# Kernel optimization log

Hardware: AMD Instinct MI355X
Metric: run time of the kernel (lower is better)

## Reference

```python
import jax, jax.numpy as jnp
import numpy as np

E = 512   # embed_dim == decoder_dim (structurally required by the module)
D = 512
V = 10000
B = 64
S = 32    # encoded caption length; max decode steps T = S - 1


def _lstm_cell(x, h, c, wih, whh, bih, bhh):
    # torch.nn.LSTMCell gate order: i, f, g, o
    gates = x @ wih.T + h @ whh.T + bih + bhh
    i, f, g, o = jnp.split(gates, 4, axis=-1)
    c2 = jax.nn.sigmoid(f) * c + jax.nn.sigmoid(i) * jnp.tanh(g)
    h2 = jax.nn.sigmoid(o) * jnp.tanh(c2)
    return h2, c2


def setup_inputs() -> dict:
    key = jax.random.key(0)
    ks = jax.random.split(key, 16)
    encoder_out = jax.random.normal(ks[0], (B, E), jnp.float32)
    encoded_captions = jax.random.randint(ks[1], (B, S), 0, V)
    # lengths sorted descending (required by the ragged :batch_size_t slicing); force max = S
    lens = np.sort(np.asarray(jax.random.randint(ks[2], (B,), 8, S + 1)))[::-1].copy()
    lens[0] = S
    caption_lengths = jnp.asarray(lens, jnp.int32)
    u = lambda k, sh: jax.random.uniform(k, sh, jnp.float32, -0.1, 0.1)
    return {
        'encoder_out': encoder_out,
        'encoded_captions': encoded_captions,
        'caption_lengths': caption_lengths,
        'embedding': u(ks[3], (V, E)),
        'dec_wih': u(ks[4], (4 * D, 2 * E)),
        'dec_whh': u(ks[5], (4 * D, D)),
        'dec_bih': u(ks[6], (4 * D,)),
        'dec_bhh': u(ks[7], (4 * D,)),
        'w_wih': u(ks[8], (4, E)),
        'w_whh': u(ks[9], (4, 1)),
        'w_bih': u(ks[10], (4,)),
        'w_bhh': u(ks[11], (4,)),
        'init_h_w': u(ks[12], (1, E)),
        'init_h_b': jnp.zeros((1,), jnp.float32),
        'init_c_w': u(ks[13], (1, E)),
        'init_c_b': jnp.zeros((1,), jnp.float32),
        'cls_w': u(ks[14], (V, D)),
        'cls_b': jnp.zeros((V,), jnp.float32),
    }


def reference(encoder_out, encoded_captions, caption_lengths, embedding,
              dec_wih, dec_whh, dec_bih, dec_bhh,
              w_wih, w_whh, w_bih, w_bhh,
              init_h_w, init_h_b, init_c_w, init_c_b,
              cls_w, cls_b):
    dl = caption_lengths - 1                      # decode lengths, [B]
    T = int(np.max(np.asarray(dl)))
    emb = embedding[encoded_captions]             # [B,S,E]
    xs = jnp.moveaxis(emb[:, :T, :], 1, 0)        # [T,B,E]
    wh0 = encoder_out @ init_h_w.T + init_h_b     # [B,1]
    wc0 = encoder_out @ init_c_w.T + init_c_b     # [B,1]

    def step(carry, inp):
        t, x_e = inp
        h, c, wh, wc = carry
        m = (dl > t).astype(x_e.dtype)[:, None]   # [B,1] active-row mask (ragged batch)
        wh2, wc2 = _lstm_cell(encoder_out, wh, wc, w_wih, w_whh, w_bih, w_bhh)
        x = jnp.concatenate([x_e, encoder_out], axis=-1)           # [B,2E]
        h2, c2 = _lstm_cell(x, h, c, dec_wih, dec_whh, dec_bih, dec_bhh)
        preds = (h2 @ cls_w.T + cls_b) * m        # inactive rows stay 0 (dropout is eval-mode identity)
        wgt = jax.nn.sigmoid(wh2)[:, 0] * m[:, 0] # [B]
        keep = m > 0
        carry = (jnp.where(keep, h2, h), jnp.where(keep, c2, c),
                 jnp.where(keep, wh2, wh), jnp.where(keep, wc2, wc))
        return carry, (preds, wgt)

    carry0 = (encoder_out, encoder_out, wh0, wc0)
    _, (p_seq, w_seq) = jax.lax.scan(step, carry0, (jnp.arange(T), xs))
    predictions = jnp.moveaxis(p_seq, 0, 1)                        # [B,T,V]
    weights = jnp.broadcast_to(w_seq.T[:, :, None], (B, T, V))     # replicate per-step scalar across vocab
    return predictions, dl, weights
```

## Files before the change

kernel.cpp:

```cpp
#include <hip/hip_runtime.h>
#include <hip/hip_bf16.h>


typedef __attribute__((ext_vector_type(4))) float f32x4;
typedef __attribute__((ext_vector_type(8))) short short8;
typedef __attribute__((ext_vector_type(4))) unsigned short u16x4;

#define BB 64
#define SS 32
#define TT 31
#define EE 512
#define VV 10000

__device__ __forceinline__ float sigf(float x){ return 1.0f/(1.0f + __expf(-x)); }
__device__ __forceinline__ float tanh_(float x){
  x = fminf(15.f, fmaxf(-15.f, x));
  float e = __expf(2.f*x);
  return (e-1.f)/(e+1.f);
}
__device__ __forceinline__ unsigned short f2bf(float x){
  __hip_bfloat16 h = __float2bfloat16(x);
  return __builtin_bit_cast(unsigned short, h);
}
__device__ __forceinline__ short8 cvt8(f32x4 a, f32x4 b){
  short8 t;
  t[0] = (short)f2bf(a.x); t[1] = (short)f2bf(a.y);
  t[2] = (short)f2bf(a.z); t[3] = (short)f2bf(a.w);
  t[4] = (short)f2bf(b.x); t[5] = (short)f2bf(b.y);
  t[6] = (short)f2bf(b.z); t[7] = (short)f2bf(b.w);
  return t;
}
__device__ __forceinline__ short8 ld16_coh(const void* p){
  short8 r;
  asm volatile("global_load_dwordx4 %0, %1, off sc0 sc1" : "=v"(r) : "v"(p) : "memory");
  return r;
}
__device__ __forceinline__ void st8_coh(void* p, unsigned long long v){
  asm volatile("global_store_dwordx2 %0, %1, off sc0 sc1" :: "v"(p), "v"(v) : "memory");
}

#define NPREP 2048
__global__ __launch_bounds__(256) void k_prep(
    const float* __restrict__ dwih, const float* __restrict__ dwhh,
    const float* __restrict__ emb, const int* __restrict__ cap,
    const float* __restrict__ enc,
    __hip_bfloat16* __restrict__ wihbf, __hip_bfloat16* __restrict__ whhbf,
    __hip_bfloat16* __restrict__ xa, __hip_bfloat16* __restrict__ h0,
    const int* __restrict__ caplen,
    const float* __restrict__ wwih, const float* __restrict__ wwhh,
    const float* __restrict__ wbih, const float* __restrict__ wbhh,
    const float* __restrict__ ihw, const float* __restrict__ ihb,
    const float* __restrict__ icw, const float* __restrict__ icb,
    float* __restrict__ wgt, unsigned* __restrict__ flags,
    float* __restrict__ dl_out)
{
  if (blockIdx.x >= NPREP){
    int b = blockIdx.x - NPREP;
    int w = threadIdx.x >> 6, lane = threadIdx.x & 63;
    __shared__ float sv[6];

    float p = 0.f;
    for (int k = lane; k < EE; k += 64) p += enc[b*EE + k] * wwih[w*EE + k];
    #pragma unroll
    for (int off = 32; off; off >>= 1) p += __shfl_down(p, off, 64);
    if (lane == 0) sv[w] = p;

    if (w < 2){
      const float* iw = (w == 0) ? ihw : icw;
      float q = 0.f;
      for (int k = lane; k < EE; k += 64) q += enc[b*EE + k] * iw[k];
      #pragma unroll
      for (int off = 32; off; off >>= 1) q += __shfl_down(q, off, 64);
      if (lane == 0) sv[4 + w] = q + ((w == 0) ? ihb[0] : icb[0]);
    }
    __syncthreads();

    if (threadIdx.x == 0){
      float wh = sv[4], wc = sv[5];
      int dl = caplen[b] - 1;
      for (int t = 0; t < TT; t++){
        float gi = sv[0] + wh*wwhh[0] + wbih[0] + wbhh[0];
        float gf = sv[1] + wh*wwhh[1] + wbih[1] + wbhh[1];
        float gg = sv[2] + wh*wwhh[2] + wbih[2] + wbhh[2];
        float go = sv[3] + wh*wwhh[3] + wbih[3] + wbhh[3];
        float wc2 = sigf(gf)*wc + sigf(gi)*tanh_(gg);
        float wh2 = sigf(go)*tanh_(wc2);
        float m = (dl > t) ? 1.f : 0.f;
        wgt[b*TT + t] = sigf(wh2) * m;
        if (dl > t){ wh = wh2; wc = wc2; }
      }
      dl_out[b] = (float)dl;
    }
    if (b == 0) for (int i = threadIdx.x; i < 4096; i += 256) flags[i] = 0;
    return;
  }

  const int n1 = 262144;
  const int n2 = n1 + 131072;
  const int n3 = n2 + 253952;
  const int n4 = n3 + 4096;
  for (int i = blockIdx.x*blockDim.x + threadIdx.x; i < n4; i += NPREP*256){
    const float* src; __hip_bfloat16* dst;
    if (i < n1){ src = dwih + (size_t)i*8; dst = wihbf + (size_t)i*8; }
    else if (i < n2){ int j = i - n1; src = dwhh + (size_t)j*8; dst = whhbf + (size_t)j*8; }
    else if (i < n3){
      int j = i - n2; int e = j*8;
      int r = e >> 10, k = e & 1023, t = r >> 6, b = r & 63;
      src = (k < 512) ? emb + (size_t)cap[b*SS + t]*EE + k
                      : enc + (size_t)b*EE + (k - 512);
      dst = xa + (size_t)e;
    } else {
      int j = i - n3; int e = j*8;
      src = enc + (size_t)e; dst = h0 + (size_t)e;
    }
    f32x4 lo = *(const f32x4*)src;
    f32x4 hi = *(const f32x4*)(src + 4);
    *(short8*)dst = cvt8(lo, hi);
  }
}

__global__ __launch_bounds__(256) void k_xproj(
    const __hip_bfloat16* __restrict__ xa, const __hip_bfloat16* __restrict__ wihbf,
    const float* __restrict__ bih, const float* __restrict__ bhh,
    float* __restrict__ xp)
{
  int bm = blockIdx.y;
  int bn = blockIdx.x;
  int w = threadIdx.x >> 6, lane = threadIdx.x & 63;
  int col = lane & 15, kg = lane >> 4;
  int m0 = bm*64;
  int n0 = bn*256 + w*64;

  f32x4 acc[4][4] = {};
  for (int kk = 0; kk < 32; kk++){
    short8 aW[4], aX[4];
    #pragma unroll
    for (int i = 0; i < 4; i++){
      aW[i] = *(const short8*)(wihbf + (size_t)(n0 + i*16 + col)*1024 + kk*32 + kg*8);
      aX[i] = *(const short8*)(xa    + (size_t)(m0 + i*16 + col)*1024 + kk*32 + kg*8);
    }
    #pragma unroll
    for (int nt = 0; nt < 4; nt++)
      #pragma unroll
      for (int mt = 0; mt < 4; mt++)
        acc[nt][mt] = __builtin_amdgcn_mfma_f32_16x16x32_bf16(aW[nt], aX[mt], acc[nt][mt], 0, 0, 0);
  }
  #pragma unroll
  for (int nt = 0; nt < 4; nt++){
    int n = n0 + nt*16 + 4*kg;
    f32x4 badd = *(const f32x4*)(bih + n);
    f32x4 b2   = *(const f32x4*)(bhh + n);
    badd = badd + b2;
    #pragma unroll
    for (int mt = 0; mt < 4; mt++){
      int r = m0 + mt*16 + col;
      *(f32x4*)(xp + (size_t)r*2048 + n) = acc[nt][mt] + badd;
    }
  }
}

__global__ __launch_bounds__(64, 1) void k_rec(
    const __hip_bfloat16* __restrict__ whhbf,
    const float* __restrict__ xp,
    const float* __restrict__ enc,
    const int* __restrict__ caplen,
    char* __restrict__ hbuf,
    __hip_bfloat16* __restrict__ hout,
    unsigned* __restrict__ flags,
    const float* __restrict__ clsw,
    __hip_bfloat16* __restrict__ clsbf)
{
  const int bid = blockIdx.x;
  const int lane = threadIdx.x;

  if (bid >= 128){
    const int n4 = 1280000;
    for (int i = (bid - 128)*64 + lane; i < n4; i += 384*64){
      f32x4 v = ((const f32x4*)clsw)[i];
      u16x4 o;
      o.x = f2bf(v.x); o.y = f2bf(v.y); o.z = f2bf(v.z); o.w = f2bf(v.w);
      ((u16x4*)clsbf)[i] = o;
    }
    return;
  }

  const int g = bid >> 5, s = bid & 31;
  const int col = lane & 15, kg = lane >> 4;
  const int d0 = s*16;
  const int b  = g*16 + col;
  const int dbase = d0 + 4*kg;
  const int pme = (dbase >> 2);

  short8 Aq[4][16];
  #pragma unroll
  for (int q = 0; q < 4; q++){
    const __hip_bfloat16* wrow = whhbf + (size_t)(q*512 + d0 + col)*512;
    #pragma unroll
    for (int kk = 0; kk < 16; kk++)
      Aq[q][kk] = *(const short8*)(wrow + kk*32 + kg*8);
  }
  #pragma unroll
  for (int q = 0; q < 4; q++)
    #pragma unroll
    for (int kk = 0; kk < 16; kk++)
      asm volatile("" : "+v"(Aq[q][kk]));

  float hst[4], cst[4];
  #pragma unroll
  for (int j = 0; j < 4; j++){
    float e0 = enc[(size_t)b*EE + dbase + j];
    hst[j] = e0; cst[j] = e0;
  }
  const int dl = caplen[b] - 1;
  unsigned* myflag = flags + (size_t)(g*32 + s)*32;
  const unsigned* pollflag = flags + (size_t)(g*32 + (lane & 31))*32;

  f32x4 xg[4];
  #pragma unroll
  for (int q = 0; q < 4; q++)
    xg[q] = *(const f32x4*)(xp + (size_t)b*2048 + q*512 + dbase);

  for (int t = 0; t < TT; t++){
    if (t > 0){
      const unsigned tgt = (unsigned)t;
      while (1){
        unsigned v = __hip_atomic_load(pollflag, __ATOMIC_RELAXED, __HIP_MEMORY_SCOPE_AGENT);
        v = min(v, (unsigned)__shfl_xor((int)v, 1, 64));
        v = min(v, (unsigned)__shfl_xor((int)v, 2, 64));
        v = min(v, (unsigned)__shfl_xor((int)v, 4, 64));
        v = min(v, (unsigned)__shfl_xor((int)v, 8, 64));
        v = min(v, (unsigned)__shfl_xor((int)v, 16, 64));
        if (v >= tgt) break;
        __builtin_amdgcn_s_sleep(1);
      }
    }

    const char* hc = hbuf + (size_t)(t & 1)*65536 + (size_t)b*1024 + kg*16;
    short8 Bf[16];
    #pragma unroll
    for (int kk = 0; kk < 16; kk++)
      Bf[kk] = ld16_coh(hc + kk*64);

    f32x4 xgn[4];
    if (t + 1 < TT){
      #pragma unroll
      for (int q = 0; q < 4; q++)
        xgn[q] = *(const f32x4*)(xp + (size_t)((t+1)*BB + b)*2048 + q*512 + dbase);
    }

    asm volatile("s_waitcnt vmcnt(0)" ::: "memory");
    __builtin_amdgcn_sched_barrier(0);

    f32x4 acc[4] = {};
    #pragma unroll
    for (int kk = 0; kk < 16; kk++)
      #pragma unroll
      for (int q = 0; q < 4; q++)
        acc[q] = __builtin_amdgcn_mfma_f32_16x16x32_bf16(Aq[q][kk], Bf[kk], acc[q], 0, 0, 0);

    const bool act = dl > t;
    unsigned long long hpack = 0, spack = 0;
    #pragma unroll
    for (int j = 0; j < 4; j++){
      float gi = acc[0][j] + xg[0][j];
      float gf = acc[1][j] + xg[1][j];
      float gg = acc[2][j] + xg[2][j];
      float go = acc[3][j] + xg[3][j];
      float c2 = sigf(gf)*cst[j] + sigf(gi)*tanh_(gg);
      float h2 = sigf(go)*tanh_(c2);
      if (act){ cst[j] = c2; hst[j] = h2; }
      hpack |= (unsigned long long)f2bf(h2)     << (16*j);
      spack |= (unsigned long long)f2bf(hst[j]) << (16*j);
    }

    ((unsigned long long*)hout)[((size_t)b*TT + t)*128 + pme] = hpack;

    if (t < TT - 1){
      st8_coh(hbuf + (size_t)((t + 1) & 1)*65536 + (size_t)b*1024 + (size_t)dbase*2, spack);
      asm volatile("s_waitcnt vmcnt(0)" ::: "memory");
      if (lane == 0)
        __hip_atomic_store(myflag, (unsigned)(t + 1),
                           __ATOMIC_RELAXED, __HIP_MEMORY_SCOPE_AGENT);
    }

    #pragma unroll
    for (int q = 0; q < 4; q++) xg[q] = xgn[q];
  }
}

__global__ __launch_bounds__(256) void k_cls(
    const __hip_bfloat16* __restrict__ hbf,
    const __hip_bfloat16* __restrict__ wbf,
    const float* __restrict__ clsb,
    const float* __restrict__ wgt,
    float* __restrict__ preds, float* __restrict__ wout)
{
  int bid = blockIdx.x;
  if (bid >= 1264){
    int r = bid - 1264;
    float wv = wgt[r];
    f32x4 wq = {wv, wv, wv, wv};
    f32x4* dst = (f32x4*)(wout + (size_t)r*VV);
    #pragma unroll 2
    for (int i = threadIdx.x; i < VV/4; i += 256)
      dst[i] = wq;
    return;
  }

  int bn = bid % 79, bm = bid / 79;
  int w = threadIdx.x >> 6, lane = threadIdx.x & 63;
  int col = lane & 15, kg = lane >> 4;
  int m0 = bm*128 + (w >> 1)*64;
  int n0 = bn*128 + (w & 1)*64;
  if (m0 >= 1984) return;

  int arow[4], brow[4];
  #pragma unroll
  for (int i = 0; i < 4; i++){
    arow[i] = min(m0 + i*16 + col, 1983);
    brow[i] = min(n0 + i*16 + col, 9999);
  }
  f32x4 acc[4][4] = {};
  for (int kk = 0; kk < 16; kk++){
    short8 a[4], b[4];
    #pragma unroll
    for (int i = 0; i < 4; i++){
      a[i] = *(const short8*)(hbf + (size_t)arow[i]*512 + kk*32 + kg*8);
      b[i] = *(const short8*)(wbf + (size_t)brow[i]*512 + kk*32 + kg*8);
    }
    #pragma unroll
    for (int mt = 0; mt < 4; mt++)
      #pragma unroll
      for (int nt = 0; nt < 4; nt++)
        acc[mt][nt] = __builtin_amdgcn_mfma_f32_16x16x32_bf16(a[mt], b[nt], acc[mt][nt], 0, 0, 0);
  }
  float cb[4]; int vcol[4]; bool vok[4];
  #pragma unroll
  for (int nt = 0; nt < 4; nt++){
    int v = n0 + nt*16 + col; vcol[nt] = v; vok[nt] = (v < VV);
    cb[nt] = vok[nt] ? clsb[v] : 0.f;
  }
  #pragma unroll
  for (int mt = 0; mt < 4; mt++)
    #pragma unroll
    for (int rg = 0; rg < 4; rg++){
      int r = m0 + mt*16 + 4*kg + rg;
      if (r >= 1984) continue;
      float wv = wgt[r];
      float mf = (wv > 0.f) ? 1.f : 0.f;
      size_t base = (size_t)r*VV;
      #pragma unroll
      for (int nt = 0; nt < 4; nt++){
        if (!vok[nt]) continue;
        preds[base + vcol[nt]] = (acc[mt][nt][rg] + cb[nt]) * mf;
      }
    }
}

extern "C" void kernel_launch(void* const* d_in, const int* in_sizes, int n_in,
                              void* d_out, int out_size, void* d_ws, size_t ws_size,
                              hipStream_t stream) {
  const float* enc    = (const float*)d_in[0];
  const int*   cap    = (const int*)  d_in[1];
  const int*   caplen = (const int*)  d_in[2];
  const float* emb    = (const float*)d_in[3];
  const float* dwih   = (const float*)d_in[4];
  const float* dwhh   = (const float*)d_in[5];
  const float* dbih   = (const float*)d_in[6];
  const float* dbhh   = (const float*)d_in[7];
  const float* wwih   = (const float*)d_in[8];
  const float* wwhh   = (const float*)d_in[9];
  const float* wbih   = (const float*)d_in[10];
  const float* wbhh   = (const float*)d_in[11];
  const float* ihw    = (const float*)d_in[12];
  const float* ihb    = (const float*)d_in[13];
  const float* icw    = (const float*)d_in[14];
  const float* icb    = (const float*)d_in[15];
  const float* clsw   = (const float*)d_in[16];
  const float* clsb   = (const float*)d_in[17];

  float* preds  = (float*)d_out;
  float* dl_out = preds + (size_t)BB*TT*VV;
  float* wout   = dl_out + BB;

  char* ws = (char*)d_ws;
  float*          wgt   = (float*)         (ws + 0);
  unsigned*       flags = (unsigned*)      (ws + 8192);
  __hip_bfloat16* clsbf = (__hip_bfloat16*)(ws + 24576);
  __hip_bfloat16* wihbf = (__hip_bfloat16*)(ws + 10264576);
  __hip_bfloat16* whhbf = (__hip_bfloat16*)(ws + 14458880);
  __hip_bfloat16* xa    = (__hip_bfloat16*)(ws + 16556032);
  float*          xp    = (float*)         (ws + 20619264);
  char*           hbuf  = (char*)          (ws + 36872192);
  __hip_bfloat16* hout  = (__hip_bfloat16*)(ws + 37003264);

  k_prep <<<NPREP + BB, 256, 0, stream>>>(dwih, dwhh, emb, cap, enc,
                                          wihbf, whhbf, xa,
                                          (__hip_bfloat16*)hbuf,
                                          caplen, wwih, wwhh, wbih, wbhh,
                                          ihw, ihb, icw, icb, wgt, flags, dl_out);
  k_xproj<<<dim3(8, 31), 256, 0, stream>>>(xa, wihbf, dbih, dbhh, xp);
  k_rec  <<<512, 64, 0, stream>>>(whhbf, xp, enc, caplen, hbuf, hout, flags,
                                  clsw, clsbf);
  k_cls  <<<1264 + 1984, 256, 0, stream>>>(hout, clsbf, clsb, wgt, preds, wout);
}
```

Baseline: 284.1 us.

## Stage classifier GEMM tiles through padded LDS with register prefetch

The classifier GEMM now loads 128x64 bf16 tiles of the activations and weights cooperatively into padded shared memory, then reads MFMA fragments from LDS instead of each wave fetching its own fragments straight from global memory. The next K-slice is prefetched into registers while the current one is computed. This cuts redundant global loads across waves and gives more coalesced access, at the cost of two barriers per K-step and more LDS use. The early return for out-of-range waves moves after the loop, since every thread now has to reach the barriers.

New measurement: 258.3 us. 1.1x faster.

```diff
diff --git a/kernel.cpp b/kernel.cpp
--- a/kernel.cpp
+++ b/kernel.cpp
@@ -307,38 +307,71 @@
     return;
   }
 
+  __shared__ __hip_bfloat16 Ab[128*72];
+  __shared__ __hip_bfloat16 Bb[128*72];
+
   int bn = bid % 79, bm = bid / 79;
-  int w = threadIdx.x >> 6, lane = threadIdx.x & 63;
+  int tid = threadIdx.x;
+  int w = tid >> 6, lane = tid & 63;
   int col = lane & 15, kg = lane >> 4;
+
+  int srow[4], skseg[4]; const __hip_bfloat16 *gA[4], *gB[4];
+  #pragma unroll
+  for (int j = 0; j < 4; j++){
+    int s = j*256 + tid;
+    srow[j] = s & 127; skseg[j] = s >> 7;
+    gA[j] = hbf + (size_t)min(bm*128 + srow[j], 1983)*512 + skseg[j]*8;
+    gB[j] = wbf + (size_t)min(bn*128 + srow[j], 9999)*512 + skseg[j]*8;
+  }
+
+  f32x4 acc[4][4] = {};
+  short8 rA[4], rB[4];
+  #pragma unroll
+  for (int j = 0; j < 4; j++){
+    rA[j] = *(const short8*)(gA[j]);
+    rB[j] = *(const short8*)(gB[j]);
+  }
+
+  for (int bk = 0; bk < 8; bk++){
+    __syncthreads();
+    #pragma unroll
+    for (int j = 0; j < 4; j++){
+      *(short8*)(Ab + srow[j]*72 + skseg[j]*8) = rA[j];
+      *(short8*)(Bb + srow[j]*72 + skseg[j]*8) = rB[j];
+    }
+    __syncthreads();
+    if (bk < 7){
+      #pragma unroll
+      for (int j = 0; j < 4; j++){
+        rA[j] = *(const short8*)(gA[j] + (bk+1)*64);
+        rB[j] = *(const short8*)(gB[j] + (bk+1)*64);
+      }
+    }
+    #pragma unroll
+    for (int kk2 = 0; kk2 < 2; kk2++){
+      short8 a[4], b[4];
+      #pragma unroll
+      for (int i = 0; i < 4; i++){
+        int ra = (w >> 1)*64 + i*16 + col;
+        int rb = (w & 1)*64 + i*16 + col;
+        a[i] = *(const short8*)(Ab + ra*72 + kk2*32 + kg*8);
+        b[i] = *(const short8*)(Bb + rb*72 + kk2*32 + kg*8);
+      }
+      #pragma unroll
+      for (int mt = 0; mt < 4; mt++)
+        #pragma unroll
+        for (int nt = 0; nt < 4; nt++)
+          acc[mt][nt] = __builtin_amdgcn_mfma_f32_16x16x32_bf16(a[mt], b[nt], acc[mt][nt], 0, 0, 0);
+    }
+  }
+
   int m0 = bm*128 + (w >> 1)*64;
   int n0 = bn*128 + (w & 1)*64;
-  if (m0 >= 1984) return;
-
-  int arow[4], brow[4];
-  #pragma unroll
-  for (int i = 0; i < 4; i++){
-    arow[i] = min(m0 + i*16 + col, 1983);
-    brow[i] = min(n0 + i*16 + col, 9999);
-  }
-  f32x4 acc[4][4] = {};
-  for (int kk = 0; kk < 16; kk++){
-    short8 a[4], b[4];
-    #pragma unroll
-    for (int i = 0; i < 4; i++){
-      a[i] = *(const short8*)(hbf + (size_t)arow[i]*512 + kk*32 + kg*8);
-      b[i] = *(const short8*)(wbf + (size_t)brow[i]*512 + kk*32 + kg*8);
-    }
-    #pragma unroll
-    for (int mt = 0; mt < 4; mt++)
-      #pragma unroll
-      for (int nt = 0; nt < 4; nt++)
-        acc[mt][nt] = __builtin_amdgcn_mfma_f32_16x16x32_bf16(a[mt], b[nt], acc[mt][nt], 0, 0, 0);
-  }
   float cb[4]; int vcol[4]; bool vok[4];
   #pragma unroll
   for (int nt = 0; nt < 4; nt++){
     int v = n0 + nt*16 + col; vcol[nt] = v; vok[nt] = (v < VV);
-    cb[nt] = vok[nt] ? clsb[v] : 0.f;
+    cb[nt] = vok[nt] ? clsb[min(v, VV - 1)] : 0.f;
   }
   #pragma unroll
   for (int mt = 0; mt < 4; mt++)
```

## Stage GEMM tiles through LDS with register prefetch in xproj and classifier

Applied to the files above, without the earlier changes.

Both the input-projection and classifier GEMMs now stage their operand tiles through padded shared memory and use register double-buffering to prefetch the next K-slice. Per-block tiles are enlarged: xproj covers 512 columns per block and the classifier covers a 128x256 tile. Each loaded element is then reused across more warps, which cuts redundant global and L2 traffic. The trade-off is fewer blocks, higher register pressure from the larger accumulator arrays, and two barriers per K step.

Measured after the change: 258.4 us. 1.1x faster.

```diff
diff --git a/kernel.cpp b/kernel.cpp
--- a/kernel.cpp
+++ b/kernel.cpp
@@ -124,30 +124,63 @@
     const float* __restrict__ bih, const float* __restrict__ bhh,
     float* __restrict__ xp)
 {
+  __shared__ __hip_bfloat16 Wb[512*40];
+  __shared__ __hip_bfloat16 Xb[64*40];
+
   int bm = blockIdx.y;
   int bn = blockIdx.x;
-  int w = threadIdx.x >> 6, lane = threadIdx.x & 63;
+  int tid = threadIdx.x;
+  int w = tid >> 6, lane = tid & 63;
   int col = lane & 15, kg = lane >> 4;
   int m0 = bm*64;
-  int n0 = bn*256 + w*64;
-
-  f32x4 acc[4][4] = {};
-  for (int kk = 0; kk < 32; kk++){
-    short8 aW[4], aX[4];
-    #pragma unroll
-    for (int i = 0; i < 4; i++){
-      aW[i] = *(const short8*)(wihbf + (size_t)(n0 + i*16 + col)*1024 + kk*32 + kg*8);
-      aX[i] = *(const short8*)(xa    + (size_t)(m0 + i*16 + col)*1024 + kk*32 + kg*8);
-    }
-    #pragma unroll
-    for (int nt = 0; nt < 4; nt++)
+
+  int wrow[8], wseg[8];
+  const __hip_bfloat16* gW[8];
+  #pragma unroll
+  for (int j = 0; j < 8; j++){
+    int s = j*256 + tid;
+    wrow[j] = s >> 2; wseg[j] = s & 3;
+    gW[j] = wihbf + (size_t)(bn*512 + wrow[j])*1024 + wseg[j]*8;
+  }
+  int xrow = tid >> 2, xseg = tid & 3;
+  const __hip_bfloat16* gX = xa + (size_t)(m0 + xrow)*1024 + xseg*8;
+
+  f32x4 acc[8][4] = {};
+  short8 rW[8], rX;
+  #pragma unroll
+  for (int j = 0; j < 8; j++) rW[j] = *(const short8*)(gW[j]);
+  rX = *(const short8*)(gX);
+
+  for (int bk = 0; bk < 32; bk++){
+    __syncthreads();
+    #pragma unroll
+    for (int j = 0; j < 8; j++)
+      *(short8*)(Wb + wrow[j]*40 + wseg[j]*8) = rW[j];
+    *(short8*)(Xb + xrow*40 + xseg*8) = rX;
+    __syncthreads();
+    if (bk < 31){
+      #pragma unroll
+      for (int j = 0; j < 8; j++)
+        rW[j] = *(const short8*)(gW[j] + (bk+1)*32);
+      rX = *(const short8*)(gX + (bk+1)*32);
+    }
+    short8 aW[8], aX[4];
+    #pragma unroll
+    for (int i = 0; i < 8; i++)
+      aW[i] = *(const short8*)(Wb + (w*128 + i*16 + col)*40 + kg*8);
+    #pragma unroll
+    for (int i = 0; i < 4; i++)
+      aX[i] = *(const short8*)(Xb + (i*16 + col)*40 + kg*8);
+    #pragma unroll
+    for (int nt = 0; nt < 8; nt++)
       #pragma unroll
       for (int mt = 0; mt < 4; mt++)
         acc[nt][mt] = __builtin_amdgcn_mfma_f32_16x16x32_bf16(aW[nt], aX[mt], acc[nt][mt], 0, 0, 0);
   }
-  #pragma unroll
-  for (int nt = 0; nt < 4; nt++){
-    int n = n0 + nt*16 + 4*kg;
+
+  #pragma unroll
+  for (int nt = 0; nt < 8; nt++){
+    int n = bn*512 + w*128 + nt*16 + 4*kg;
     f32x4 badd = *(const f32x4*)(bih + n);
     f32x4 b2   = *(const f32x4*)(bhh + n);
     badd = badd + b2;
@@ -296,8 +329,8 @@
     float* __restrict__ preds, float* __restrict__ wout)
 {
   int bid = blockIdx.x;
-  if (bid >= 1264){
-    int r = bid - 1264;
+  if (bid >= 640){
+    int r = bid - 640;
     float wv = wgt[r];
     f32x4 wq = {wv, wv, wv, wv};
     f32x4* dst = (f32x4*)(wout + (size_t)r*VV);
@@ -307,38 +340,72 @@
     return;
   }
 
-  int bn = bid % 79, bm = bid / 79;
-  int w = threadIdx.x >> 6, lane = threadIdx.x & 63;
+  __shared__ __hip_bfloat16 Ab[128*40];
+  __shared__ __hip_bfloat16 Bb[256*40];
+
+  int bn = bid % 40, bm = bid / 40;
+  int tid = threadIdx.x;
+  int w = tid >> 6, lane = tid & 63;
   int col = lane & 15, kg = lane >> 4;
+
+  int arow[2], aseg[2]; const __hip_bfloat16* gA[2];
+  #pragma unroll
+  for (int j = 0; j < 2; j++){
+    int s = j*256 + tid;
+    arow[j] = s >> 2; aseg[j] = s & 3;
+    gA[j] = hbf + (size_t)min(bm*128 + arow[j], 1983)*512 + aseg[j]*8;
+  }
+  int brow[4], bseg[4]; const __hip_bfloat16* gB[4];
+  #pragma unroll
+  for (int j = 0; j < 4; j++){
+    int s = j*256 + tid;
+    brow[j] = s >> 2; bseg[j] = s & 3;
+    gB[j] = wbf + (size_t)min(bn*256 + brow[j], 9999)*512 + bseg[j]*8;
+  }
+
+  f32x4 acc[4][8] = {};
+  short8 rA[2], rB[4];
+  #pragma unroll
+  for (int j = 0; j < 2; j++) rA[j] = *(const short8*)(gA[j]);
+  #pragma unroll
+  for (int j = 0; j < 4; j++) rB[j] = *(const short8*)(gB[j]);
+
+  for (int bk = 0; bk < 16; bk++){
+    __syncthreads();
+    #pragma unroll
+    for (int j = 0; j < 2; j++)
+      *(short8*)(Ab + arow[j]*40 + aseg[j]*8) = rA[j];
+    #pragma unroll
+    for (int j = 0; j < 4; j++)
+      *(short8*)(Bb + brow[j]*40 + bseg[j]*8) = rB[j];
+    __syncthreads();
+    if (bk < 15){
+      #pragma unroll
+      for (int j = 0; j < 2; j++) rA[j] = *(const short8*)(gA[j] + (bk+1)*32);
+      #pragma unroll
+      for (int j = 0; j < 4; j++) rB[j] = *(const short8*)(gB[j] + (bk+1)*32);
+    }
+    short8 a[4], b[8];
+    #pragma unroll
+    for (int i = 0; i < 4; i++)
+      a[i] = *(const short8*)(Ab + ((w >> 1)*64 + i*16 + col)*40 + kg*8);
+    #pragma unroll
+    for (int i = 0; i < 8; i++)
+      b[i] = *(const short8*)(Bb + ((w & 1)*128 + i*16 + col)*40 + kg*8);
+    #pragma unroll
+    for (int mt = 0; mt < 4; mt++)
+      #pragma unroll
+      for (int nt = 0; nt < 8; nt++)
+        acc[mt][nt] = __builtin_amdgcn_mfma_f32_16x16x32_bf16(a[mt], b[nt], acc[mt][nt], 0, 0, 0);
+  }
+
   int m0 = bm*128 + (w >> 1)*64;
-  int n0 = bn*128 + (w & 1)*64;
-  if (m0 >= 1984) return;
-
-  int arow[4], brow[4];
-  #pragma unroll
-  for (int i = 0; i < 4; i++){
-    arow[i] = min(m0 + i*16 + col, 1983);
-    brow[i] = min(n0 + i*16 + col, 9999);
-  }
-  f32x4 acc[4][4] = {};
-  for (int kk = 0; kk < 16; kk++){
-    short8 a[4], b[4];
-    #pragma unroll
-    for (int i = 0; i < 4; i++){
-      a[i] = *(const short8*)(hbf + (size_t)arow[i]*512 + kk*32 + kg*8);
-      b[i] = *(const short8*)(wbf + (size_t)brow[i]*512 + kk*32 + kg*8);
-    }
-    #pragma unroll
-    for (int mt = 0; mt < 4; mt++)
-      #pragma unroll
-      for (int nt = 0; nt < 4; nt++)
-        acc[mt][nt] = __builtin_amdgcn_mfma_f32_16x16x32_bf16(a[mt], b[nt], acc[mt][nt], 0, 0, 0);
-  }
-  float cb[4]; int vcol[4]; bool vok[4];
-  #pragma unroll
-  for (int nt = 0; nt < 4; nt++){
+  int n0 = bn*256 + (w & 1)*128;
+  float cb[8]; int vcol[8]; bool vok[8];
+  #pragma unroll
+  for (int nt = 0; nt < 8; nt++){
     int v = n0 + nt*16 + col; vcol[nt] = v; vok[nt] = (v < VV);
-    cb[nt] = vok[nt] ? clsb[v] : 0.f;
+    cb[nt] = vok[nt] ? clsb[min(v, VV - 1)] : 0.f;
   }
   #pragma unroll
   for (int mt = 0; mt < 4; mt++)
@@ -350,7 +417,7 @@
       float mf = (wv > 0.f) ? 1.f : 0.f;
       size_t base = (size_t)r*VV;
       #pragma unroll
-      for (int nt = 0; nt < 4; nt++){
+      for (int nt = 0; nt < 8; nt++){
         if (!vok[nt]) continue;
         preds[base + vcol[nt]] = (acc[mt][nt][rg] + cb[nt]) * mf;
       }
@@ -399,8 +466,8 @@
                                           (__hip_bfloat16*)hbuf,
                                           caplen, wwih, wwhh, wbih, wbhh,
                                           ihw, ihb, icw, icb, wgt, flags, dl_out);
-  k_xproj<<<dim3(8, 31), 256, 0, stream>>>(xa, wihbf, dbih, dbhh, xp);
+  k_xproj<<<dim3(4, 31), 256, 0, stream>>>(xa, wihbf, dbih, dbhh, xp);
   k_rec  <<<512, 64, 0, stream>>>(whhbf, xp, enc, caplen, hbuf, hout, flags,
                                   clsw, clsbf);
-  k_cls  <<<1264 + 1984, 256, 0, stream>>>(hout, clsbf, clsb, wgt, preds, wout);
-}
+  k_cls  <<<640 + 1984, 256, 0, stream>>>(hout, clsbf, clsb, wgt, preds, wout);
+}
```
